# Kernel optimization log

Hardware: AMD Instinct MI355X
Metric: run time of the kernel (lower is better)

Reference implementation:

```python
import jax, jax.numpy as jnp
import numpy as np
import math

N_QUBITS = 8
N_QLAYERS = 3
B, C, H, W = 32, 128, 128, 128
SH, SW = H // 2, W // 2
FLAT = C * SH * SW  # 524288


def setup_inputs() -> dict:
    key = jax.random.key(0)
    ks = jax.random.split(key, 8)
    x = jax.random.normal(ks[0], (B, C, H, W), jnp.float32)
    s_in = 1.0 / math.sqrt(FLAT)
    q_in_W = jax.random.uniform(ks[1], (4, N_QUBITS, FLAT), jnp.float32, -s_in, s_in)
    q_in_b = jax.random.uniform(ks[2], (4, N_QUBITS), jnp.float32, -s_in, s_in)
    q_weights = jax.random.uniform(ks[3], (4, N_QLAYERS, N_QUBITS, 3), jnp.float32, 0.0, 2.0 * math.pi)
    s_out = 1.0 / math.sqrt(N_QUBITS)
    q_out_W = jax.random.uniform(ks[4], (4, FLAT, N_QUBITS), jnp.float32, -s_out, s_out)
    q_out_b = jax.random.uniform(ks[5], (4, FLAT), jnp.float32, -s_out, s_out)
    s_f = 1.0 / math.sqrt(C)
    fuse_W = jax.random.uniform(ks[6], (C, C), jnp.float32, -s_f, s_f)
    fuse_b = jax.random.uniform(ks[7], (C,), jnp.float32, -s_f, s_f)
    return dict(x=x, q_in_W=q_in_W, q_in_b=q_in_b, q_weights=q_weights,
                q_out_W=q_out_W, q_out_b=q_out_b, fuse_W=fuse_W, fuse_b=fuse_b)


def _apply_1q_batched(st, U, q):
    # st: (B, 2,...,2); U: (B,2,2) per-sample gate on wire q
    st2 = jnp.moveaxis(st, q + 1, 1)
    out = jnp.einsum('bij,bj...->bi...', U, st2)
    return jnp.moveaxis(out, 1, q + 1)


def _apply_1q_shared(st, U, q):
    # U: (2,2) shared gate on wire q
    st2 = jnp.moveaxis(st, q + 1, 1)
    out = jnp.einsum('ij,bj...->bi...', U, st2)
    return jnp.moveaxis(out, 1, q + 1)


def _cnot(st, c, t):
    # flip target axis where control == 1
    st2 = jnp.moveaxis(st, (c + 1, t + 1), (1, 2))
    out = jnp.stack([st2[:, 0], st2[:, 1, ::-1]], axis=1)
    return jnp.moveaxis(out, (1, 2), (c + 1, t + 1))


def _rx(a):
    # AngleEmbedding default rotation is RX; a: (B,) -> (B,2,2) complex
    c = jnp.cos(a / 2)
    s = jnp.sin(a / 2)
    return jnp.stack([jnp.stack([c + 0j, -1j * s], -1),
                      jnp.stack([-1j * s, c + 0j], -1)], -2)


def _rot(phi, theta, omega):
    # PennyLane Rot = RZ(omega) RY(theta) RZ(phi) -> (2,2) complex
    ct = jnp.cos(theta / 2)
    st_ = jnp.sin(theta / 2)
    ep = jnp.exp(-0.5j * (phi + omega))
    em = jnp.exp(-0.5j * (phi - omega))
    row0 = jnp.stack([ep * ct, -jnp.conj(em) * st_])
    row1 = jnp.stack([em * st_, jnp.conj(ep) * ct])
    return jnp.stack([row0, row1])


def quantum_expvals(angles, weights):
    # angles: (B, n); weights: (L, n, 3) -> (B, n) PauliZ expvals
    n = N_QUBITS
    Bq = angles.shape[0]
    state = jnp.zeros((Bq, 2 ** n), jnp.complex64).at[:, 0].set(1.0)
    state = state.reshape((Bq,) + (2,) * n)
    for q in range(n):
        state = _apply_1q_batched(state, _rx(angles[:, q]), q)
    for l in range(N_QLAYERS):
        for q in range(n):
            state = _apply_1q_shared(state, _rot(weights[l, q, 0], weights[l, q, 1], weights[l, q, 2]), q)
        for q in range(n - 1):
            state = _cnot(state, q, q + 1)
        state = _cnot(state, n - 1, 0)
    probs = jnp.abs(state) ** 2
    ev = []
    for q in range(n):
        axes = tuple(i for i in range(1, n + 1) if i != q + 1)
        p = probs.sum(axes)  # (B, 2)
        ev.append(p[:, 0] - p[:, 1])
    return jnp.stack(ev, axis=1)


def _dwt_haar(x):
    a = x[..., 0::2, 0::2]
    b = x[..., 0::2, 1::2]
    c = x[..., 1::2, 0::2]
    d = x[..., 1::2, 1::2]
    ll = (a + b + c + d) * 0.5
    lh = (a + b - c - d) * 0.5
    hl = (a - b + c - d) * 0.5
    hh = (a - b - c + d) * 0.5
    return ll, lh, hl, hh


def _idwt_haar(ll, lh, hl, hh):
    a = (ll + lh + hl + hh) * 0.5
    b = (ll + lh - hl - hh) * 0.5
    c = (ll - lh + hl - hh) * 0.5
    d = (ll - lh - hl + hh) * 0.5
    Bq, Cq, h, w = ll.shape
    top = jnp.stack([a, b], axis=-1).reshape(Bq, Cq, h, 2 * w)
    bot = jnp.stack([c, d], axis=-1).reshape(Bq, Cq, h, 2 * w)
    return jnp.stack([top, bot], axis=-2).reshape(Bq, Cq, 2 * h, 2 * w)


def _qlayer(y, W_in, b_in, qw, W_out, b_out):
    # y: (B, FLAT)
    q_in = y @ W_in.T + b_in            # (B, n_qubits)
    ev = quantum_expvals(q_in, qw)       # (B, n_qubits)
    return ev @ W_out.T + b_out          # (B, FLAT)


def reference(x, q_in_W, q_in_b, q_weights, q_out_W, q_out_b, fuse_W, fuse_b):
    Bq = x.shape[0]
    ll, lh, hl, hh = _dwt_haar(x)
    sub_shape = ll.shape
    subs = jnp.stack([ll, lh, hl, hh], 0).reshape(4, Bq, -1)  # (4, B, FLAT)
    proc = jax.vmap(_qlayer)(subs, q_in_W, q_in_b, q_weights, q_out_W, q_out_b)
    pl = proc.reshape((4,) + sub_shape)
    rec = _idwt_haar(pl[0], pl[1], pl[2], pl[3])
    fused = jnp.einsum('bchw,oc->bohw', rec, fuse_W) + fuse_b[None, :, None, None]
    return x + fused
```

## Files before the change

### kernel.cpp

```cpp
#include <hip/hip_runtime.h>

#define NB 32
#define NC 128
#define NH 128
#define NW 128
#define SH 64
#define SW 64
#define FLAT (NC*SH*SW)

__device__ __forceinline__ float2 cmul(float2 a, float2 b) {
    return make_float2(a.x*b.x - a.y*b.y, a.x*b.y + a.y*b.x);
}

__global__ void k0_init_qin(const float* __restrict__ q_in_b, float* __restrict__ qin) {
    int idx = blockIdx.x*256 + threadIdx.x;
    if (idx < 1024) {
        int k = idx >> 8, q = idx & 7;
        qin[idx] = q_in_b[k*8 + q];
    }
}

__global__ __launch_bounds__(512) void k1_qin(const float* __restrict__ x,
                                              const float* __restrict__ qw,
                                              float* __restrict__ qin) {
    int c    = blockIdx.x;
    int bg   = blockIdx.y;
    int wave = threadIdx.x >> 6;
    int lane = threadIdx.x & 63;
    int b    = bg*8 + wave;
    const float* xb = x  + (size_t)(b*NC + c) * (NH*NW);
    const float* Wc = qw + (size_t)c * (SH*SW);
    float acc[32];
    #pragma unroll
    for (int t = 0; t < 32; t++) acc[t] = 0.f;
    for (int i = 0; i < 64; i++) {
        const float* xr = xb + (2*i)*NW + 2*lane;
        float2 t0 = *(const float2*)xr;
        float2 t1 = *(const float2*)(xr + NW);
        float s0 = (t0.x + t0.y + t1.x + t1.y)*0.5f;
        float s1 = (t0.x + t0.y - t1.x - t1.y)*0.5f;
        float s2 = (t0.x - t0.y + t1.x - t1.y)*0.5f;
        float s3 = (t0.x - t0.y - t1.x + t1.y)*0.5f;
        int fo = i*64 + lane;
        #pragma unroll
        for (int k = 0; k < 4; k++) {
            float s = (k==0) ? s0 : (k==1) ? s1 : (k==2) ? s2 : s3;
            #pragma unroll
            for (int q = 0; q < 8; q++)
                acc[k*8+q] += s * Wc[(size_t)(k*8+q)*FLAT + fo];
        }
    }
    #pragma unroll
    for (int t = 0; t < 32; t++) {
        float v = acc[t];
        #pragma unroll
        for (int off = 32; off >= 1; off >>= 1) v += __shfl_down(v, off, 64);
        if (lane == 0)
            atomicAdd(&qin[(t>>3)*256 + b*8 + (t&7)], v);
    }
}

__global__ __launch_bounds__(256) void k2_qsim(const float* __restrict__ qin,
                                               const float* __restrict__ qweights,
                                               float* __restrict__ ev) {
    int k = blockIdx.x >> 5, b = blockIdx.x & 31;
    int tid = threadIdx.x;
    __shared__ float2 st[256];
    __shared__ float  pr[256];
    __shared__ float  ang[8];
    if (tid < 8) ang[tid] = qin[(k*32+b)*8 + tid];
    st[tid] = make_float2(tid == 0 ? 1.f : 0.f, 0.f);
    __syncthreads();
    for (int q = 0; q < 8; q++) {
        int bp = 7-q;
        float h = 0.5f*ang[q];
        float cA = cosf(h), sA = sinf(h);
        float2 self = st[tid];
        float2 part = st[tid ^ (1<<bp)];
        float2 nv = make_float2(cA*self.x + sA*part.y, cA*self.y - sA*part.x);
        __syncthreads(); st[tid] = nv; __syncthreads();
    }
    for (int l = 0; l < 3; l++) {
        for (int q = 0; q < 8; q++) {
            const float* w = qweights + ((k*3 + l)*8 + q)*3;
            float phi = w[0], th = w[1], om = w[2];
            float ct = cosf(0.5f*th), sst = sinf(0.5f*th);
            float ap = -0.5f*(phi+om), am = -0.5f*(phi-om);
            float cp = cosf(ap), sp = sinf(ap), cm = cosf(am), sm = sinf(am);
            float2 U00 = make_float2( cp*ct,  sp*ct);
            float2 U01 = make_float2(-cm*sst, sm*sst);
            float2 U10 = make_float2( cm*sst, sm*sst);
            float2 U11 = make_float2( cp*ct, -sp*ct);
            int bp = 7-q;
            int bit = (tid>>bp)&1;
            float2 self = st[tid], part = st[tid ^ (1<<bp)];
            float2 m0, m1;
            if (bit == 0) { m0 = cmul(U00, self); m1 = cmul(U01, part); }
            else          { m0 = cmul(U10, part); m1 = cmul(U11, self); }
            float2 nv = make_float2(m0.x + m1.x, m0.y + m1.y);
            __syncthreads(); st[tid] = nv; __syncthreads();
        }
        for (int q = 0; q < 7; q++) {
            int bc = 7-q, bt = 6-q;
            float2 v = ((tid>>bc)&1) ? st[tid ^ (1<<bt)] : st[tid];
            __syncthreads(); st[tid] = v; __syncthreads();
        }
        {
            int bc = 0, bt = 7;
            float2 v = ((tid>>bc)&1) ? st[tid ^ (1<<bt)] : st[tid];
            __syncthreads(); st[tid] = v; __syncthreads();
        }
    }
    pr[tid] = st[tid].x*st[tid].x + st[tid].y*st[tid].y;
    __syncthreads();
    if (tid < 8) {
        int bp = 7 - tid;
        float s = 0.f;
        for (int i = 0; i < 256; i++) s += ((i>>bp)&1) ? -pr[i] : pr[i];
        ev[(k*32+b)*8 + tid] = s;
    }
}

__global__ __launch_bounds__(256) void k3_gemmG(const float* __restrict__ q_out_W,
                                                const float* __restrict__ q_out_b,
                                                const float* __restrict__ fuse_W,
                                                float* __restrict__ Gb,
                                                float* __restrict__ G) {
    int k = blockIdx.x / 288;
    int r = blockIdx.x % 288;
    const float* Bg; float* Og; int ldB; int n0;
    if (r < 256) { n0 = r*128;       Bg = q_out_W + (size_t)k*4194304; ldB = 32768; Og = G  + (size_t)k*4194304; }
    else         { n0 = (r-256)*128; Bg = q_out_b + (size_t)k*FLAT;    ldB = 4096;  Og = Gb + (size_t)k*FLAT; }
    __shared__ float As[32*132];
    __shared__ float Bs[32*132];
    int tid = threadIdx.x;
    int ty = tid >> 4, tx = tid & 15;
    float acc[8][8];
    #pragma unroll
    for (int m = 0; m < 8; m++)
        #pragma unroll
        for (int n = 0; n < 8; n++) acc[m][n] = 0.f;
    for (int c0 = 0; c0 < 128; c0 += 32) {
        for (int idx = tid; idx < 32*128; idx += 256) {
            int o = idx >> 5, cc = idx & 31;
            As[cc*132 + o] = fuse_W[o*128 + c0 + cc];
        }
        for (int idx = tid; idx < 32*128; idx += 256) {
            int cc = idx >> 7, n = idx & 127;
            Bs[cc*132 + n] = Bg[(size_t)(c0+cc)*ldB + n0 + n];
        }
        __syncthreads();
        #pragma unroll 2
        for (int cc = 0; cc < 32; cc++) {
            float4 a0 = *(const float4*)&As[cc*132 + ty*8];
            float4 a1 = *(const float4*)&As[cc*132 + ty*8 + 4];
            float4 b0 = *(const float4*)&Bs[cc*132 + tx*8];
            float4 b1 = *(const float4*)&Bs[cc*132 + tx*8 + 4];
            float av[8] = {a0.x,a0.y,a0.z,a0.w,a1.x,a1.y,a1.z,a1.w};
            float bv[8] = {b0.x,b0.y,b0.z,b0.w,b1.x,b1.y,b1.z,b1.w};
            #pragma unroll
            for (int m = 0; m < 8; m++)
                #pragma unroll
                for (int n = 0; n < 8; n++) acc[m][n] += av[m]*bv[n];
        }
        __syncthreads();
    }
    #pragma unroll
    for (int mm = 0; mm < 8; mm++) {
        int m = ty*8 + mm;
        float* orow = Og + (size_t)m*ldB + n0 + tx*8;
        *(float4*)orow       = make_float4(acc[mm][0], acc[mm][1], acc[mm][2], acc[mm][3]);
        *(float4*)(orow + 4) = make_float4(acc[mm][4], acc[mm][5], acc[mm][6], acc[mm][7]);
    }
}

__global__ __launch_bounds__(256) void k4_epilogue(const float* __restrict__ x,
                                                   const float* __restrict__ ev,
                                                   const float* __restrict__ Gb,
                                                   const float* __restrict__ G,
                                                   const float* __restrict__ fuse_b,
                                                   float* __restrict__ out) {
    int i    = blockIdx.x;
    int o    = blockIdx.y;
    int lane = threadIdx.x & 63;
    int wg   = threadIdx.x >> 6;
    float4 g[4][2]; float gb[4];
    #pragma unroll
    for (int k = 0; k < 4; k++) {
        const float* gp = G + ((size_t)((k*128+o)*4096) + i*64 + lane)*8;
        g[k][0] = *(const float4*)gp;
        g[k][1] = *(const float4*)(gp + 4);
        gb[k]   = Gb[(size_t)(k*128+o)*4096 + i*64 + lane];
    }
    float fb = fuse_b[o];
    for (int bi = 0; bi < 8; bi++) {
        int b = wg*8 + bi;
        float T[4];
        #pragma unroll
        for (int k = 0; k < 4; k++) {
            const float* e = ev + (k*32+b)*8;
            float4 e0 = *(const float4*)e;
            float4 e1 = *(const float4*)(e + 4);
            T[k] = gb[k]
                 + e0.x*g[k][0].x + e0.y*g[k][0].y + e0.z*g[k][0].z + e0.w*g[k][0].w
                 + e1.x*g[k][1].x + e1.y*g[k][1].y + e1.z*g[k][1].z + e1.w*g[k][1].w;
        }
        float pa = 0.5f*(T[0]+T[1]+T[2]+T[3]) + fb;
        float pb = 0.5f*(T[0]+T[1]-T[2]-T[3]) + fb;
        float pc = 0.5f*(T[0]-T[1]+T[2]-T[3]) + fb;
        float pd = 0.5f*(T[0]-T[1]-T[2]+T[3]) + fb;
        size_t base = ((size_t)(b*128 + o)*128 + 2*i)*128 + 2*lane;
        float2 x0 = *(const float2*)(x + base);
        float2 x1 = *(const float2*)(x + base + 128);
        *(float2*)(out + base)       = make_float2(x0.x + pa, x0.y + pb);
        *(float2*)(out + base + 128) = make_float2(x1.x + pc, x1.y + pd);
    }
}

extern "C" void kernel_launch(void* const* d_in, const int* in_sizes, int n_in,
                              void* d_out, int out_size, void* d_ws, size_t ws_size,
                              hipStream_t stream) {
    const float* x         = (const float*)d_in[0];
    const float* q_in_W    = (const float*)d_in[1];
    const float* q_in_b    = (const float*)d_in[2];
    const float* q_weights = (const float*)d_in[3];
    const float* q_out_W   = (const float*)d_in[4];
    const float* q_out_b   = (const float*)d_in[5];
    const float* fuse_W    = (const float*)d_in[6];
    const float* fuse_b    = (const float*)d_in[7];
    float* out = (float*)d_out;

    float* wsf = (float*)d_ws;
    float* qin = wsf;
    float* ev  = wsf + 1024;
    float* Gb  = wsf + 2048;
    float* G   = wsf + 2048 + 4*128*4096;

    k0_init_qin<<<4, 256, 0, stream>>>(q_in_b, qin);
    k1_qin<<<dim3(128, 4), 512, 0, stream>>>(x, q_in_W, qin);
    k2_qsim<<<128, 256, 0, stream>>>(qin, q_weights, ev);
    k3_gemmG<<<1152, 256, 0, stream>>>(q_out_W, q_out_b, fuse_W, Gb, G);
    k4_epilogue<<<dim3(64, 128), 256, 0, stream>>>(x, ev, Gb, G, fuse_b, out);
}
```

Measured before the change: 882.6 us.

## Restructure k1_qin: two batches per wave, float4 loads, split rows across z

The input-projection kernel now has each wave process two batch samples at once, so every weight float4 load is reused for both samples, and each lane loads four columns with vectorized float4 reads. Rows are split across a new z grid dimension, which doubles the number of blocks. The final reduction uses xor shuffles and a single atomic per lane instead of 32 atomics from lane 0. Register pressure rises with two 32-entry accumulators, and there are twice as many atomics on qin in total.

Result: faster. 785.4 us (-11.0%).

```diff
diff --git a/kernel.cpp b/kernel.cpp
--- a/kernel.cpp
+++ b/kernel.cpp
@@ -20,44 +20,86 @@
     }
 }
 
-__global__ __launch_bounds__(512) void k1_qin(const float* __restrict__ x,
-                                              const float* __restrict__ qw,
-                                              float* __restrict__ qin) {
+__global__ __launch_bounds__(256, 2) void k1_qin(const float* __restrict__ x,
+                                                 const float* __restrict__ qw,
+                                                 float* __restrict__ qin) {
     int c    = blockIdx.x;
     int bg   = blockIdx.y;
+    int ic   = blockIdx.z;
     int wave = threadIdx.x >> 6;
     int lane = threadIdx.x & 63;
-    int b    = bg*8 + wave;
-    const float* xb = x  + (size_t)(b*NC + c) * (NH*NW);
-    const float* Wc = qw + (size_t)c * (SH*SW);
-    float acc[32];
-    #pragma unroll
-    for (int t = 0; t < 32; t++) acc[t] = 0.f;
-    for (int i = 0; i < 64; i++) {
-        const float* xr = xb + (2*i)*NW + 2*lane;
-        float2 t0 = *(const float2*)xr;
-        float2 t1 = *(const float2*)(xr + NW);
-        float s0 = (t0.x + t0.y + t1.x + t1.y)*0.5f;
-        float s1 = (t0.x + t0.y - t1.x - t1.y)*0.5f;
-        float s2 = (t0.x - t0.y + t1.x - t1.y)*0.5f;
-        float s3 = (t0.x - t0.y - t1.x + t1.y)*0.5f;
-        int fo = i*64 + lane;
-        #pragma unroll
-        for (int k = 0; k < 4; k++) {
-            float s = (k==0) ? s0 : (k==1) ? s1 : (k==2) ? s2 : s3;
-            #pragma unroll
-            for (int q = 0; q < 8; q++)
-                acc[k*8+q] += s * Wc[(size_t)(k*8+q)*FLAT + fo];
-        }
-    }
+    int b0   = bg*8 + wave*2;
+    int lr   = lane >> 4;
+    int lj   = (lane & 15) << 2;
+
+    const float* xb0 = x + (size_t)(b0*NC + c) * (NH*NW);
+    const float* xb1 = xb0 + (size_t)NC*NH*NW;
+    const float* Wb  = qw + (size_t)c * (SH*SW);
+
+    float acc0[32], acc1[32];
+    #pragma unroll
+    for (int t = 0; t < 32; t++) { acc0[t] = 0.f; acc1[t] = 0.f; }
+
+    #pragma unroll 1
+    for (int it = 0; it < 8; it++) {
+        int i    = ic*32 + it*4 + lr;
+        int xoff = (2*i)*NW + 2*lj;
+
+        float4 t00 = *(const float4*)(xb0 + xoff);
+        float4 t01 = *(const float4*)(xb0 + xoff + 4);
+        float4 t10 = *(const float4*)(xb0 + xoff + NW);
+        float4 t11 = *(const float4*)(xb0 + xoff + NW + 4);
+        float4 u00 = *(const float4*)(xb1 + xoff);
+        float4 u01 = *(const float4*)(xb1 + xoff + 4);
+        float4 u10 = *(const float4*)(xb1 + xoff + NW);
+        float4 u11 = *(const float4*)(xb1 + xoff + NW + 4);
+
+        float s0[4][4], s1[4][4];
+        {
+            float tp, tm, bp, bm;
+            tp = t00.x + t00.y; tm = t00.x - t00.y; bp = t10.x + t10.y; bm = t10.x - t10.y;
+            s0[0][0] = tp + bp; s0[1][0] = tp - bp; s0[2][0] = tm + bm; s0[3][0] = tm - bm;
+            tp = t00.z + t00.w; tm = t00.z - t00.w; bp = t10.z + t10.w; bm = t10.z - t10.w;
+            s0[0][1] = tp + bp; s0[1][1] = tp - bp; s0[2][1] = tm + bm; s0[3][1] = tm - bm;
+            tp = t01.x + t01.y; tm = t01.x - t01.y; bp = t11.x + t11.y; bm = t11.x - t11.y;
+            s0[0][2] = tp + bp; s0[1][2] = tp - bp; s0[2][2] = tm + bm; s0[3][2] = tm - bm;
+            tp = t01.z + t01.w; tm = t01.z - t01.w; bp = t11.z + t11.w; bm = t11.z - t11.w;
+            s0[0][3] = tp + bp; s0[1][3] = tp - bp; s0[2][3] = tm + bm; s0[3][3] = tm - bm;
+            tp = u00.x + u00.y; tm = u00.x - u00.y; bp = u10.x + u10.y; bm = u10.x - u10.y;
+            s1[0][0] = tp + bp; s1[1][0] = tp - bp; s1[2][0] = tm + bm; s1[3][0] = tm - bm;
+            tp = u00.z + u00.w; tm = u00.z - u00.w; bp = u10.z + u10.w; bm = u10.z - u10.w;
+            s1[0][1] = tp + bp; s1[1][1] = tp - bp; s1[2][1] = tm + bm; s1[3][1] = tm - bm;
+            tp = u01.x + u01.y; tm = u01.x - u01.y; bp = u11.x + u11.y; bm = u11.x - u11.y;
+            s1[0][2] = tp + bp; s1[1][2] = tp - bp; s1[2][2] = tm + bm; s1[3][2] = tm - bm;
+            tp = u01.z + u01.w; tm = u01.z - u01.w; bp = u11.z + u11.w; bm = u11.z - u11.w;
+            s1[0][3] = tp + bp; s1[1][3] = tp - bp; s1[2][3] = tm + bm; s1[3][3] = tm - bm;
+        }
+
+        const float* wp = Wb + (size_t)(i*64 + lj);
+        #pragma unroll
+        for (int kq = 0; kq < 32; kq++) {
+            float4 w = *(const float4*)(wp + (size_t)kq*FLAT);
+            int k = kq >> 3;
+            acc0[kq] += s0[k][0]*w.x + s0[k][1]*w.y + s0[k][2]*w.z + s0[k][3]*w.w;
+            acc1[kq] += s1[k][0]*w.x + s1[k][1]*w.y + s1[k][2]*w.z + s1[k][3]*w.w;
+        }
+    }
+
+    float myv = 0.f;
     #pragma unroll
     for (int t = 0; t < 32; t++) {
-        float v = acc[t];
-        #pragma unroll
-        for (int off = 32; off >= 1; off >>= 1) v += __shfl_down(v, off, 64);
-        if (lane == 0)
-            atomicAdd(&qin[(t>>3)*256 + b*8 + (t&7)], v);
-    }
+        float v0 = acc0[t], v1 = acc1[t];
+        #pragma unroll
+        for (int off = 32; off >= 1; off >>= 1) {
+            v0 += __shfl_xor(v0, off, 64);
+            v1 += __shfl_xor(v1, off, 64);
+        }
+        if (lane == t)      myv = v0;
+        if (lane == t + 32) myv = v1;
+    }
+    int t  = lane & 31;
+    int bb = b0 + (lane >> 5);
+    atomicAdd(&qin[(t>>3)*256 + bb*8 + (t&7)], 0.5f*myv);
 }
 
 __global__ __launch_bounds__(256) void k2_qsim(const float* __restrict__ qin,
@@ -237,7 +279,7 @@
     float* G   = wsf + 2048 + 4*128*4096;
 
     k0_init_qin<<<4, 256, 0, stream>>>(q_in_b, qin);
-    k1_qin<<<dim3(128, 4), 512, 0, stream>>>(x, q_in_W, qin);
+    k1_qin<<<dim3(128, 4, 2), 256, 0, stream>>>(x, q_in_W, qin);
     k2_qsim<<<128, 256, 0, stream>>>(qin, q_weights, ev);
     k3_gemmG<<<1152, 256, 0, stream>>>(q_out_W, q_out_b, fuse_W, Gb, G);
     k4_epilogue<<<dim3(64, 128), 256, 0, stream>>>(x, ev, Gb, G, fuse_b, out);
```
